# Optimization experiments

Measured on AMD Instinct MI355X. Metric: run time of the kernel, lower is better.

The kernel has to match this reference:

```python
import jax, jax.numpy as jnp
import numpy as np

S, R, CM, H, CA, CZ = 128, 256, 256, 8, 32, 128


def _ln(x, w, b):
    mu = x.mean(-1, keepdims=True)
    var = x.var(-1, keepdims=True)
    return (x - mu) * jax.lax.rsqrt(var + 1e-5) * w + b


def setup_inputs() -> dict:
    key = jax.random.key(0)
    ks = jax.random.split(key, 20)
    n = lambda i, shape: jax.random.normal(ks[i], shape, jnp.float32) * 0.05
    return {
        "m": jax.random.normal(ks[0], (S, R, CM), jnp.float32),
        "m_mask": jnp.ones((S, R), jnp.float32),
        "z": jax.random.normal(ks[1], (R, R, CZ), jnp.float32),
        "row_ln_w": jnp.ones((CM,)), "row_ln_b": jnp.zeros((CM,)),
        "row_z_ln_w": jnp.ones((CZ,)), "row_z_ln_b": jnp.zeros((CZ,)),
        "row_wq": n(2, (CM, H * CA)), "row_wk": n(3, (CM, H * CA)), "row_wv": n(4, (CM, H * CA)),
        "row_wb": n(5, (CZ, H)),
        "row_wg": n(6, (CM, H * CA)), "row_bg": jnp.zeros((H * CA,)),
        "row_wo": n(7, (H * CA, CM)), "row_bo": jnp.zeros((CM,)),
        "col_ln_w": jnp.ones((CM,)), "col_ln_b": jnp.zeros((CM,)),
        "col_wq": n(8, (CM, H * CA)), "col_wk": n(9, (CM, H * CA)), "col_wv": n(10, (CM, H * CA)),
        "col_wg": n(11, (CM, H * CA)), "col_bg": jnp.zeros((H * CA,)),
        "col_wo": n(12, (H * CA, CM)), "col_bo": jnp.zeros((CM,)),
        "tr_ln_w": jnp.ones((CM,)), "tr_ln_b": jnp.zeros((CM,)),
        "tr_w1": n(13, (CM, 4 * CM)), "tr_b1": jnp.zeros((4 * CM,)),
        "tr_w2": n(14, (4 * CM, CM)), "tr_b2": jnp.zeros((CM,)),
    }


def _row_atten(m, m_mask, z, ln_w, ln_b, z_ln_w, z_ln_b, wq, wk, wv, wb, wg, bg, wo, bo):
    # MSA row attention with pair bias: attend over residues within each sequence row.
    x = _ln(m, ln_w, ln_b)                                   # [s,r,cm]
    q = (x @ wq).reshape(S, R, H, CA) * (CA ** -0.5)
    k = (x @ wk).reshape(S, R, H, CA)
    v = (x @ wv).reshape(S, R, H, CA)
    pair_bias = jnp.transpose(_ln(z, z_ln_w, z_ln_b) @ wb, (2, 0, 1))  # [h,r,r]
    mask_bias = (m_mask - 1.0)[:, None, None, :] * 1e9       # [s,1,1,r] over keys
    logits = jnp.einsum('sqhc,skhc->shqk', q, k) + pair_bias[None] + mask_bias
    a = jax.nn.softmax(logits, axis=-1)
    o = jnp.einsum('shqk,skhc->sqhc', a, v)
    g = jax.nn.sigmoid(x @ wg + bg).reshape(S, R, H, CA)
    return (g * o).reshape(S, R, H * CA) @ wo + bo


def _col_atten(m, m_mask, ln_w, ln_b, wq, wk, wv, wg, bg, wo, bo):
    # MSA column attention: attend over sequences within each residue column.
    x = _ln(m, ln_w, ln_b)                                   # [s,r,cm]
    q = (x @ wq).reshape(S, R, H, CA) * (CA ** -0.5)
    k = (x @ wk).reshape(S, R, H, CA)
    v = (x @ wv).reshape(S, R, H, CA)
    mask_bias = (jnp.transpose(m_mask) - 1.0)[:, None, None, :] * 1e9  # [r,1,1,s]
    logits = jnp.einsum('qrhc,krhc->rhqk', q, k) + mask_bias
    a = jax.nn.softmax(logits, axis=-1)
    o = jnp.einsum('rhqk,krhc->qrhc', a, v)
    g = jax.nn.sigmoid(x @ wg + bg).reshape(S, R, H, CA)
    return (g * o).reshape(S, R, H * CA) @ wo + bo


def _transition(m, ln_w, ln_b, w1, b1, w2, b2):
    x = _ln(m, ln_w, ln_b)
    return jax.nn.relu(x @ w1 + b1) @ w2 + b2


def reference(m, m_mask, z,
              row_ln_w, row_ln_b, row_z_ln_w, row_z_ln_b,
              row_wq, row_wk, row_wv, row_wb, row_wg, row_bg, row_wo, row_bo,
              col_ln_w, col_ln_b, col_wq, col_wk, col_wv, col_wg, col_bg, col_wo, col_bo,
              tr_ln_w, tr_ln_b, tr_w1, tr_b1, tr_w2, tr_b2):
    m = m + _row_atten(m, m_mask, z, row_ln_w, row_ln_b, row_z_ln_w, row_z_ln_b,
                       row_wq, row_wk, row_wv, row_wb, row_wg, row_bg, row_wo, row_bo)
    m = m + _col_atten(m, m_mask, col_ln_w, col_ln_b, col_wq, col_wk, col_wv,
                       col_wg, col_bg, col_wo, col_bo)
    m = m + _transition(m, tr_ln_w, tr_ln_b, tr_w1, tr_b1, tr_w2, tr_b2)
    return m
```

## Files before the change

### kernel.cpp

```cpp
#include <hip/hip_runtime.h>
#include <stdint.h>

#define S_ 128
#define R_ 256
#define CM_ 256
#define H_ 8
#define CA_ 32
#define CZ_ 128

typedef unsigned short u16;
typedef __bf16 bf16x8 __attribute__((ext_vector_type(8)));
typedef float f32x4 __attribute__((ext_vector_type(4)));

#define LOG2E 1.4426950408889634f

__device__ __forceinline__ float bf2f(u16 u){ unsigned v = ((unsigned)u) << 16; float f; __builtin_memcpy(&f, &v, 4); return f; }
__device__ __forceinline__ u16 f2bf(float f){ __bf16 h = (__bf16)f; u16 u; __builtin_memcpy(&u, &h, 2); return u; }
__device__ __forceinline__ unsigned pkbf(float lo, float hi){
  unsigned r; asm("v_cvt_pk_bf16_f32 %0, %1, %2" : "=v"(r) : "v"(lo), "v"(hi)); return r;
}
__device__ __forceinline__ float fexp2(float x){
  float r; asm("v_exp_f32 %0, %1" : "=v"(r) : "v"(x)); return r;
}

__device__ __forceinline__ void gl16(const void* g, void* l){
  __builtin_amdgcn_global_load_lds((const __attribute__((address_space(1))) void*)g,
                                   (__attribute__((address_space(3))) void*)l, 16, 0, 0);
}

struct WSrc { const float* p[12]; };
__global__ __launch_bounds__(256) void transpose_all(WSrc srcs, u16* __restrict__ dst){
  int b = blockIdx.x, t = threadIdx.x;
  int job, idx;
  if(b < 2560){ job = b >> 8; idx = ((b & 255) << 8) + t; }
  else if(b < 3584){ job = 10; idx = ((b - 2560) << 8) + t; }
  else { job = 11; idx = ((b - 3584) << 8) + t; }
  int K = (job == 11) ? 1024 : 256;
  int N = (job == 10) ? 1024 : 256;
  int off;
  if(job < 10) off = job * 65536;
  else if(job == 10) off = 655360;
  else off = 917504;
  int k = idx / N, n = idx - k * N;
  float sc = (job == 0 || job == 5) ? (0.17677669529663687f * LOG2E) : 1.f;
  dst[off + n * K + k] = f2bf(srcs.p[job][idx] * sc);
}

template<bool BF16IN>
__global__ __launch_bounds__(256) void ln_kernel(const void* __restrict__ inv, const float* __restrict__ w,
                          const float* __restrict__ b, u16* __restrict__ out){
  int wv = threadIdx.x >> 6, lane = threadIdx.x & 63;
  long long row = (long long)blockIdx.x * 4 + wv;
  float vx, vy, vz, vw;
  if(BF16IN){
    ushort4 v4 = ((const ushort4*)((const u16*)inv + row * CM_))[lane];
    vx = bf2f(v4.x); vy = bf2f(v4.y); vz = bf2f(v4.z); vw = bf2f(v4.w);
  } else {
    float4 v4 = ((const float4*)((const float*)inv + row * CM_))[lane];
    vx = v4.x; vy = v4.y; vz = v4.z; vw = v4.w;
  }
  float s = vx + vy + vz + vw;
  for(int mo = 32; mo; mo >>= 1) s += __shfl_xor(s, mo, 64);
  float mu = s * (1.f / CM_);
  float dx = vx - mu, dy = vy - mu, dz = vz - mu, dw = vw - mu;
  float s2 = dx * dx + dy * dy + dz * dz + dw * dw;
  for(int mo = 32; mo; mo >>= 1) s2 += __shfl_xor(s2, mo, 64);
  float rstd = rsqrtf(s2 * (1.f / CM_) + 1e-5f);
  float4 w4 = ((const float4*)w)[lane];
  float4 b4 = ((const float4*)b)[lane];
  ushort4 st;
  st.x = f2bf(dx * rstd * w4.x + b4.x);
  st.y = f2bf(dy * rstd * w4.y + b4.y);
  st.z = f2bf(dz * rstd * w4.z + b4.z);
  st.w = f2bf(dw * rstd * w4.w + b4.w);
  *(ushort4*)(out + row * CM_ + lane * 4) = st;
}

__global__ __launch_bounds__(256) void pair_bias_kernel(const float* __restrict__ z, const float* __restrict__ lnw,
                                 const float* __restrict__ lnb, const float* __restrict__ wb,
                                 u16* __restrict__ pb){
  __shared__ __attribute__((aligned(16))) unsigned char Xl[32 * 256];
  __shared__ __attribute__((aligned(16))) unsigned char Wl[16 * 256];
  const int t = threadIdx.x;
  const int wv = t >> 6, lane = t & 63, l15 = lane & 15, l4 = lane >> 4;
  const int r0 = blockIdx.x * 32;

  if(t < 128){
    const float4* wr = (const float4*)(wb + t * 8);
    float4 a = wr[0], bq = wr[1];
    u16 vals[8] = {f2bf(a.x), f2bf(a.y), f2bf(a.z), f2bf(a.w),
                   f2bf(bq.x), f2bf(bq.y), f2bf(bq.z), f2bf(bq.w)};
    #pragma unroll
    for(int n = 0; n < 8; n++){
      *(u16*)(Wl + ((n * 256 + t * 2) ^ ((n & 7) << 4))) = vals[n];
      *(u16*)(Wl + (((n + 8) * 256 + t * 2) ^ ((n & 7) << 4))) = 0;
    }
  }
  {
    int row = wv * 8 + (lane >> 3);
    int c0 = (lane & 7) * 16;
    const float4* rp = (const float4*)(z + (long long)(r0 + row) * CZ_ + c0);
    float4 v0 = rp[0], v1 = rp[1], v2 = rp[2], v3 = rp[3];
    float s = v0.x + v0.y + v0.z + v0.w + v1.x + v1.y + v1.z + v1.w
            + v2.x + v2.y + v2.z + v2.w + v3.x + v3.y + v3.z + v3.w;
    s += __shfl_xor(s, 1, 64); s += __shfl_xor(s, 2, 64); s += __shfl_xor(s, 4, 64);
    float mu = s * (1.f / CZ_);
    float d[16] = {v0.x - mu, v0.y - mu, v0.z - mu, v0.w - mu,
                   v1.x - mu, v1.y - mu, v1.z - mu, v1.w - mu,
                   v2.x - mu, v2.y - mu, v2.z - mu, v2.w - mu,
                   v3.x - mu, v3.y - mu, v3.z - mu, v3.w - mu};
    float s2 = 0.f;
    #pragma unroll
    for(int i = 0; i < 16; i++) s2 += d[i] * d[i];
    s2 += __shfl_xor(s2, 1, 64); s2 += __shfl_xor(s2, 2, 64); s2 += __shfl_xor(s2, 4, 64);
    float rstd = rsqrtf(s2 * (1.f / CZ_) + 1e-5f);
    const float4* wp = (const float4*)(lnw + c0);
    const float4* bp = (const float4*)(lnb + c0);
    float x[16];
    #pragma unroll
    for(int i = 0; i < 4; i++){
      float4 w4 = wp[i], b4 = bp[i];
      x[i * 4 + 0] = d[i * 4 + 0] * rstd * w4.x + b4.x;
      x[i * 4 + 1] = d[i * 4 + 1] * rstd * w4.y + b4.y;
      x[i * 4 + 2] = d[i * 4 + 2] * rstd * w4.z + b4.z;
      x[i * 4 + 3] = d[i * 4 + 3] * rstd * w4.w + b4.w;
    }
    uint4 p0, p1;
    p0.x = pkbf(x[0], x[1]);  p0.y = pkbf(x[2], x[3]);
    p0.z = pkbf(x[4], x[5]);  p0.w = pkbf(x[6], x[7]);
    p1.x = pkbf(x[8], x[9]);  p1.y = pkbf(x[10], x[11]);
    p1.z = pkbf(x[12], x[13]); p1.w = pkbf(x[14], x[15]);
    *(uint4*)(Xl + ((row * 256 + c0 * 2) ^ ((row & 7) << 4))) = p0;
    *(uint4*)(Xl + ((row * 256 + c0 * 2 + 16) ^ ((row & 7) << 4))) = p1;
  }
  __syncthreads();
  if(wv < 2){
    f32x4 acc = {0.f, 0.f, 0.f, 0.f};
    #pragma unroll
    for(int ks = 0; ks < 4; ks++){
      int rowA = wv * 16 + l15;
      bf16x8 a = *(const bf16x8*)(Xl + ((rowA * 256 + l4 * 16 + ks * 64) ^ ((rowA & 7) << 4)));
      bf16x8 b = *(const bf16x8*)(Wl + ((l15 * 256 + l4 * 16 + ks * 64) ^ ((l15 & 7) << 4)));
      acc = __builtin_amdgcn_mfma_f32_16x16x32_bf16(a, b, acc, 0, 0, 0);
    }
    if(l15 < 8){
      #pragma unroll
      for(int r = 0; r < 4; r++){
        int rowg = r0 + wv * 16 + l4 * 4 + r;
        int q = rowg >> 8, k = rowg & 255;
        int off = (((l15 * 16 + (q >> 4)) * 16 + (k >> 4)) << 10)
                + ((((q >> 2) & 3) * 16 + (k & 15)) << 2) + (q & 3);
        pb[off] = f2bf(acc[r] * LOG2E);
      }
    }
  }
}

template<bool HAS_BIAS, bool HAS_SIG, bool RELU, int RESMODE, bool F32OUT, int OUTMODE>
__global__ __launch_bounds__(256) void gemm128(
    const u16* __restrict__ A, const u16* __restrict__ Wt,
    const float* __restrict__ bias, const void* __restrict__ res,
    void* __restrict__ outv, int M, int N, int K, int sigStart){
  __shared__ __attribute__((aligned(16))) unsigned char Ab[16384];
  __shared__ __attribute__((aligned(16))) unsigned char Bb[16384];
  const int t = threadIdx.x;
  const int wv = t >> 6, lane = t & 63, l15 = lane & 15, l4 = lane >> 4;
  const int wm = wv >> 1, wn = wv & 1;
  const unsigned flat = blockIdx.y * gridDim.x + blockIdx.x;
  const unsigned NB = gridDim.x, mper = gridDim.y >> 3;
  const unsigned xcd = flat & 7, j = flat >> 3;
  const unsigned n_blk = j % NB, m_blk = xcd * mper + j / NB;
  const long long m0 = (long long)m_blk * 128;
  const int n0 = n_blk * 128;
  const int srow = t >> 3;
  const int ksw  = ((t & 7) ^ (srow & 7)) * 8;
  const u16* Ag = A  + (m0 + srow) * (long long)K + ksw;
  const u16* Bg = Wt + (long long)(n0 + srow) * K + ksw;
  f32x4 acc[4][4] = {};
  for(int kk = 0; kk < K; kk += 64){
    #pragma unroll
    for(int i = 0; i < 4; i++){
      gl16(Ag + (long long)i * 32 * K + kk, Ab + wv * 1024 + lane * 16 + i * 4096);
      gl16(Bg + (long long)i * 32 * K + kk, Bb + wv * 1024 + lane * 16 + i * 4096);
    }
    asm volatile("s_waitcnt vmcnt(0)" ::: "memory");
    __syncthreads();
    #pragma unroll
    for(int kh = 0; kh < 2; kh++){
      bf16x8 af[4], bq[4];
      #pragma unroll
      for(int mt = 0; mt < 4; mt++){
        int rr = wm * 64 + mt * 16 + l15;
        af[mt] = *(const bf16x8*)(Ab + rr * 128 + ((kh * 64 + l4 * 16) ^ ((rr & 7) << 4)));
      }
      #pragma unroll
      for(int nt = 0; nt < 4; nt++){
        int rr = wn * 64 + nt * 16 + l15;
        bq[nt] = *(const bf16x8*)(Bb + rr * 128 + ((kh * 64 + l4 * 16) ^ ((rr & 7) << 4)));
      }
      #pragma unroll
      for(int mt = 0; mt < 4; mt++)
        #pragma unroll
        for(int nt = 0; nt < 4; nt++)
          acc[mt][nt] = __builtin_amdgcn_mfma_f32_16x16x32_bf16(af[mt], bq[nt], acc[mt][nt], 0, 0, 0);
    }
    __syncthreads();
  }
  float bnt[4]; bool sg[4];
  #pragma unroll
  for(int nt = 0; nt < 4; nt++){
    int ncol = n0 + wn * 64 + nt * 16 + l15;
    bnt[nt] = 0.f; sg[nt] = false;
    if(HAS_BIAS){
      if(HAS_SIG){ sg[nt] = (ncol >= sigStart); bnt[nt] = sg[nt] ? bias[ncol - sigStart] : 0.f; }
      else bnt[nt] = bias[ncol];
    }
  }
  #pragma unroll
  for(int mt = 0; mt < 4; mt++){
    #pragma unroll
    for(int r = 0; r < 4; r++){
      long long mrow = m0 + wm * 64 + mt * 16 + l4 * 4 + r;
      long long tok = mrow;
      if(OUTMODE == 2) tok = (((mrow & 255) << 7) | (mrow >> 8));
      #pragma unroll
      for(int nt = 0; nt < 4; nt++){
        int ncol = n0 + wn * 64 + nt * 16 + l15;
        float v = acc[mt][nt][r] + bnt[nt];
        if(HAS_SIG){ if(sg[nt]) v = 1.f / (1.f + __expf(-v)); }
        if(RELU) v = v > 0.f ? v : 0.f;
        if(RESMODE == 1) v += ((const float*)res)[mrow * N + ncol];
        if(RESMODE == 2) v += bf2f(((const u16*)res)[mrow * N + ncol]);
        long long oidx;
        if(OUTMODE == 0) oidx = mrow * N + ncol;
        else oidx = ((long long)(ncol >> 5) << 20) + tok * 32 + (ncol & 31);
        if(F32OUT) ((float*)outv)[oidx] = v;
        else       ((u16*)outv)[oidx] = f2bf(v);
      }
    }
  }
}

template<int L, bool HAS_BIAS>
__global__ __launch_bounds__(256) void atten_kernel(
    const u16* __restrict__ qg, const u16* __restrict__ kg, const u16* __restrict__ vg,
    const u16* __restrict__ gg, const u16* __restrict__ pb, const float* __restrict__ mask,
    u16* __restrict__ og,
    long long obase_in, long long obase_o, long long ostride,
    long long mbase_mul, int mstride){
  __shared__ __attribute__((aligned(16))) unsigned char smem[L * 128 + 8192];
  unsigned char* Kl = smem;
  unsigned char* Vt = smem + L * 64;
  unsigned char* Pl = smem + L * 128;

  const int t = threadIdx.x;
  const int wv = t >> 6, lane = t & 63, l15 = lane & 15, l4 = lane >> 4;
  const int h = blockIdx.x & 7;
  const int outer = blockIdx.x >> 3;
  const long long base  = ((long long)h << 20) + (long long)outer * obase_in;
  const long long baseo = (long long)outer * obase_o + h * CA_;
  const long long mb = (long long)outer * mbase_mul;
  const int KT = L / 16, NC = L / 64;

  #pragma unroll
  for(int j = 0; j < L * 4; j += 256){
    int cid = j + t;
    int row = cid >> 2, ko = cid & 3;
    int4 kv = *(const int4*)(kg + base + row * 32 + ko * 8);
    *(int4*)(Kl + ((row * 64 + ko * 16) ^ ((row & 7) << 4))) = kv;
  }
  {
    const int TPT = 256 / L;
    const int CPT = 32 / TPT;
    int tok = t / TPT, part = t - tok * TPT;
    int c0 = part * CPT;
    __attribute__((aligned(16))) u16 tmp[32];
    const u16* vp = vg + base + tok * 32 + c0;
    #pragma unroll
    for(int j2 = 0; j2 < CPT / 8; j2++) ((int4*)tmp)[j2] = *(const int4*)(vp + j2 * 8);
    int kp = (tok >> 6) * 64 + (tok & 15) * 4 + ((tok >> 4) & 3);
    #pragma unroll
    for(int ci = 0; ci < CPT; ci++){
      int c = c0 + ci;
      *(u16*)(Vt + (((c * L + kp) * 2) ^ ((c & 7) << 4))) = tmp[ci];
    }
  }
  __syncthreads();

  float mskb[L / 16];
  #pragma unroll
  for(int kt = 0; kt < KT; kt++)
    mskb[kt] = (mask[mb + (long long)(kt * 16 + l15) * mstride] - 1.f) * (1e9f * LOG2E);

  bf16x8 ones;
  #pragma unroll
  for(int j = 0; j < 8; j++) ones[j] = (__bf16)1.0f;

  unsigned char* Pw = Pl + wv * 2048;
  const int NQ = L / 4;
  #pragma unroll
  for(int qt = 0; qt < NQ / 16; qt++){
    const int qrow0 = wv * NQ + qt * 16;
    bf16x8 aq = *(const bf16x8*)(qg + base + (qrow0 + l15) * 32 + l4 * 8);
    f32x4 lac[L / 16];
    #pragma unroll
    for(int kt = 0; kt < KT; kt++){
      int kr = kt * 16 + l15;
      bf16x8 bk = *(const bf16x8*)(Kl + ((kr * 64 + l4 * 16) ^ ((kr & 7) << 4)));
      f32x4 zz = {0.f, 0.f, 0.f, 0.f};
      lac[kt] = __builtin_amdgcn_mfma_f32_16x16x32_bf16(aq, bk, zz, 0, 0, 0);
    }
    const u16* tile = HAS_BIAS ? (pb + (((h * 16 + (qrow0 >> 4)) * 16) << 10) + lane * 4) : nullptr;
    #pragma unroll
    for(int kt = 0; kt < KT; kt++){
      float mm = mskb[kt];
      if(HAS_BIAS){
        ushort4 b4 = *(const ushort4*)(tile + (kt << 10));
        lac[kt][0] = fexp2(lac[kt][0] + mm + bf2f(b4.x));
        lac[kt][1] = fexp2(lac[kt][1] + mm + bf2f(b4.y));
        lac[kt][2] = fexp2(lac[kt][2] + mm + bf2f(b4.z));
        lac[kt][3] = fexp2(lac[kt][3] + mm + bf2f(b4.w));
      } else {
        #pragma unroll
        for(int r = 0; r < 4; r++) lac[kt][r] = fexp2(lac[kt][r] + mm);
      }
    }
    f32x4 oac[2] = {{0,0,0,0},{0,0,0,0}};
    f32x4 osum = {0.f, 0.f, 0.f, 0.f};
    #pragma unroll
    for(int ch = 0; ch < NC; ch++){
      asm volatile("" ::: "memory");
      #pragma unroll
      for(int r = 0; r < 4; r++){
        int qp = l4 * 4 + r;
        uint2 pk2;
        pk2.x = pkbf(lac[ch * 4 + 0][r], lac[ch * 4 + 1][r]);
        pk2.y = pkbf(lac[ch * 4 + 2][r], lac[ch * 4 + 3][r]);
        *(uint2*)(Pw + qp * 128 + ((l15 * 8) ^ ((qp & 7) << 4))) = pk2;
      }
      asm volatile("s_waitcnt lgkmcnt(0)" ::: "memory");
      #pragma unroll
      for(int ksl = 0; ksl < 2; ksl++){
        bf16x8 ap = *(const bf16x8*)(Pw + l15 * 128 + ((ksl * 64 + l4 * 16) ^ ((l15 & 7) << 4)));
        osum = __builtin_amdgcn_mfma_f32_16x16x32_bf16(ap, ones, osum, 0, 0, 0);
        #pragma unroll
        for(int ct = 0; ct < 2; ct++){
          int c = ct * 16 + l15;
          bf16x8 bv = *(const bf16x8*)(Vt + (((c * L + ch * 64 + ksl * 32 + l4 * 8) * 2) ^ ((c & 7) << 4)));
          oac[ct] = __builtin_amdgcn_mfma_f32_16x16x32_bf16(ap, bv, oac[ct], 0, 0, 0);
        }
      }
    }
    float inv[4];
    #pragma unroll
    for(int r = 0; r < 4; r++) inv[r] = 1.f / (osum[r] + 1e-30f);
    #pragma unroll
    for(int ct = 0; ct < 2; ct++)
      #pragma unroll
      for(int r = 0; r < 4; r++){
        int qi = qrow0 + l4 * 4 + r, c = ct * 16 + l15;
        float g = bf2f(gg[base + qi * 32 + c]);
        og[baseo + (long long)qi * ostride + c] = f2bf(oac[ct][r] * inv[r] * g);
      }
  }
}

extern "C" void kernel_launch(void* const* d_in, const int* in_sizes, int n_in,
                              void* d_out, int out_size, void* d_ws, size_t ws_size,
                              hipStream_t stream){
  const float* m        = (const float*)d_in[0];
  const float* m_mask   = (const float*)d_in[1];
  const float* z        = (const float*)d_in[2];
  const float* row_ln_w = (const float*)d_in[3];
  const float* row_ln_b = (const float*)d_in[4];
  const float* row_z_ln_w = (const float*)d_in[5];
  const float* row_z_ln_b = (const float*)d_in[6];
  const float* row_bg   = (const float*)d_in[12];
  const float* row_bo   = (const float*)d_in[14];
  const float* col_ln_w = (const float*)d_in[15];
  const float* col_ln_b = (const float*)d_in[16];
  const float* col_bg   = (const float*)d_in[21];
  const float* col_bo   = (const float*)d_in[23];
  const float* tr_ln_w  = (const float*)d_in[24];
  const float* tr_ln_b  = (const float*)d_in[25];
  const float* tr_b1    = (const float*)d_in[27];
  const float* tr_b2    = (const float*)d_in[29];
  float* out = (float*)d_out;
  char* ws = (char*)d_ws;

  u16* bx  = (u16*)ws;
  u16* fq  = bx + 8388608;
  u16* t_o = fq + 33554432;
  u16* pb  = t_o + 8388608;
  u16* wt  = pb + 2097152;
  u16* m2  = fq;
  u16* h1  = fq + 8388608;

  const long long HSEC = 1ll << 20;

  WSrc srcs;
  srcs.p[0] = (const float*)d_in[7];
  srcs.p[1] = (const float*)d_in[8];
  srcs.p[2] = (const float*)d_in[9];
  srcs.p[3] = (const float*)d_in[11];
  srcs.p[4] = (const float*)d_in[13];
  srcs.p[5] = (const float*)d_in[17];
  srcs.p[6] = (const float*)d_in[18];
  srcs.p[7] = (const float*)d_in[19];
  srcs.p[8] = (const float*)d_in[20];
  srcs.p[9] = (const float*)d_in[22];
  srcs.p[10] = (const float*)d_in[26];
  srcs.p[11] = (const float*)d_in[28];

  dim3 b256(256);
  transpose_all<<<dim3(4608), b256, 0, stream>>>(srcs, wt);
  pair_bias_kernel<<<dim3(2048), b256, 0, stream>>>(z, row_z_ln_w, row_z_ln_b,
                                                    (const float*)d_in[10], pb);

  ln_kernel<false><<<dim3(8192), b256, 0, stream>>>(m, row_ln_w, row_ln_b, bx);
  gemm128<true,true,false,0,false,1><<<dim3(8,256), b256, 0, stream>>>(
      bx, wt, row_bg, nullptr, fq, 32768, 1024, 256, 768);
  atten_kernel<256,true><<<dim3(1024), b256, 0, stream>>>(
      fq, fq + 8 * HSEC, fq + 16 * HSEC, fq + 24 * HSEC, pb, m_mask, t_o,
      8192, 65536, 256, 256, 1);
  gemm128<true,false,false,1,false,0><<<dim3(2,256), b256, 0, stream>>>(
      t_o, wt + 262144, row_bo, m, bx, 32768, 256, 256, 0);

  ln_kernel<true><<<dim3(8192), b256, 0, stream>>>(bx, col_ln_w, col_ln_b, t_o);
  gemm128<true,true,false,0,false,2><<<dim3(8,256), b256, 0, stream>>>(
      t_o, wt + 327680, col_bg, nullptr, fq, 32768, 1024, 256, 768);
  atten_kernel<128,false><<<dim3(2048), b256, 0, stream>>>(
      fq, fq + 8 * HSEC, fq + 16 * HSEC, fq + 24 * HSEC, nullptr, m_mask, t_o,
      4096, 256, 65536, 1, 256);
  gemm128<true,false,false,2,false,0><<<dim3(2,256), b256, 0, stream>>>(
      t_o, wt + 589824, col_bo, bx, m2, 32768, 256, 256, 0);

  ln_kernel<true><<<dim3(8192), b256, 0, stream>>>(m2, tr_ln_w, tr_ln_b, bx);
  gemm128<true,false,true,0,false,0><<<dim3(8,256), b256, 0, stream>>>(
      bx, wt + 655360, tr_b1, nullptr, h1, 32768, 1024, 256, 0);
  gemm128<true,false,false,2,true,0><<<dim3(2,256), b256, 0, stream>>>(
      h1, wt + 917504, tr_b2, m2, out, 32768, 256, 1024, 0);
}
```

Measured before the change: 262.6 us.

## Double-buffer LDS tiles in gemm128 to overlap global loads with MFMA

The GEMM main loop now splits LDS into two buffers with a K-step of 32. The next tile's global-to-LDS loads are issued before the current tile is computed, with a partial vmcnt wait, so memory latency can overlap with MFMA work. In exchange there are twice as many loop iterations and barriers per K, and the swizzle changes to a 4-way XOR pattern. That pattern may raise LDS bank conflicts.

```diff
diff --git a/kernel.cpp b/kernel.cpp
--- a/kernel.cpp
+++ b/kernel.cpp
@@ -161,8 +161,8 @@
     const u16* __restrict__ A, const u16* __restrict__ Wt,
     const float* __restrict__ bias, const void* __restrict__ res,
     void* __restrict__ outv, int M, int N, int K, int sigStart){
-  __shared__ __attribute__((aligned(16))) unsigned char Ab[16384];
-  __shared__ __attribute__((aligned(16))) unsigned char Bb[16384];
+  __shared__ __attribute__((aligned(16))) unsigned char Ab[2][8192];
+  __shared__ __attribute__((aligned(16))) unsigned char Bb[2][8192];
   const int t = threadIdx.x;
   const int wv = t >> 6, lane = t & 63, l15 = lane & 15, l4 = lane >> 4;
   const int wm = wv >> 1, wn = wv & 1;
@@ -172,39 +172,53 @@
   const unsigned n_blk = j % NB, m_blk = xcd * mper + j / NB;
   const long long m0 = (long long)m_blk * 128;
   const int n0 = n_blk * 128;
-  const int srow = t >> 3;
-  const int ksw  = ((t & 7) ^ (srow & 7)) * 8;
-  const u16* Ag = A  + (m0 + srow) * (long long)K + ksw;
-  const u16* Bg = Wt + (long long)(n0 + srow) * K + ksw;
+  const int row0 = t >> 2, sl0 = t & 3;
+  const int row1 = row0 + 64;
+  const int ks0 = (sl0 ^ (row0 & 3)) * 8;
+  const int ks1 = (sl0 ^ (row1 & 3)) * 8;
+  const u16* Ag0 = A  + (m0 + row0) * (long long)K + ks0;
+  const u16* Ag1 = A  + (m0 + row1) * (long long)K + ks1;
+  const u16* Bg0 = Wt + (long long)(n0 + row0) * K + ks0;
+  const u16* Bg1 = Wt + (long long)(n0 + row1) * K + ks1;
+  const int lofs = t * 16;
   f32x4 acc[4][4] = {};
-  for(int kk = 0; kk < K; kk += 64){
-    #pragma unroll
-    for(int i = 0; i < 4; i++){
-      gl16(Ag + (long long)i * 32 * K + kk, Ab + wv * 1024 + lane * 16 + i * 4096);
-      gl16(Bg + (long long)i * 32 * K + kk, Bb + wv * 1024 + lane * 16 + i * 4096);
-    }
-    asm volatile("s_waitcnt vmcnt(0)" ::: "memory");
-    __syncthreads();
-    #pragma unroll
-    for(int kh = 0; kh < 2; kh++){
-      bf16x8 af[4], bq[4];
-      #pragma unroll
-      for(int mt = 0; mt < 4; mt++){
-        int rr = wm * 64 + mt * 16 + l15;
-        af[mt] = *(const bf16x8*)(Ab + rr * 128 + ((kh * 64 + l4 * 16) ^ ((rr & 7) << 4)));
-      }
-      #pragma unroll
-      for(int nt = 0; nt < 4; nt++){
-        int rr = wn * 64 + nt * 16 + l15;
-        bq[nt] = *(const bf16x8*)(Bb + rr * 128 + ((kh * 64 + l4 * 16) ^ ((rr & 7) << 4)));
-      }
-      #pragma unroll
-      for(int mt = 0; mt < 4; mt++)
-        #pragma unroll
-        for(int nt = 0; nt < 4; nt++)
-          acc[mt][nt] = __builtin_amdgcn_mfma_f32_16x16x32_bf16(af[mt], bq[nt], acc[mt][nt], 0, 0, 0);
-    }
-    __syncthreads();
+  const int nsteps = K >> 5;
+  gl16(Ag0, Ab[0] + lofs);
+  gl16(Ag1, Ab[0] + 4096 + lofs);
+  gl16(Bg0, Bb[0] + lofs);
+  gl16(Bg1, Bb[0] + 4096 + lofs);
+  int cur = 0;
+  for(int ts = 0; ts < nsteps; ts++){
+    if(ts + 1 < nsteps){
+      int kk = (ts + 1) << 5;
+      gl16(Ag0 + kk, Ab[cur ^ 1] + lofs);
+      gl16(Ag1 + kk, Ab[cur ^ 1] + 4096 + lofs);
+      gl16(Bg0 + kk, Bb[cur ^ 1] + lofs);
+      gl16(Bg1 + kk, Bb[cur ^ 1] + 4096 + lofs);
+      asm volatile("s_waitcnt vmcnt(4)" ::: "memory");
+    } else {
+      asm volatile("s_waitcnt vmcnt(0)" ::: "memory");
+    }
+    __builtin_amdgcn_s_barrier();
+    bf16x8 af[4], bq[4];
+    #pragma unroll
+    for(int mt = 0; mt < 4; mt++){
+      int rr = wm * 64 + mt * 16 + l15;
+      af[mt] = *(const bf16x8*)(Ab[cur] + rr * 64 + ((l4 * 16) ^ ((rr & 3) << 4)));
+    }
+    #pragma unroll
+    for(int nt = 0; nt < 4; nt++){
+      int rr = wn * 64 + nt * 16 + l15;
+      bq[nt] = *(const bf16x8*)(Bb[cur] + rr * 64 + ((l4 * 16) ^ ((rr & 3) << 4)));
+    }
+    #pragma unroll
+    for(int mt = 0; mt < 4; mt++)
+      #pragma unroll
+      for(int nt = 0; nt < 4; nt++)
+        acc[mt][nt] = __builtin_amdgcn_mfma_f32_16x16x32_bf16(af[mt], bq[nt], acc[mt][nt], 0, 0, 0);
+    asm volatile("s_waitcnt lgkmcnt(0)" ::: "memory");
+    __builtin_amdgcn_s_barrier();
+    cur ^= 1;
   }
   float bnt[4]; bool sg[4];
   #pragma unroll
```

New measurement: 266.2 us. About the same (+1.3%).
